# Kernel optimization log

Hardware: AMD Instinct MI355X
Metric: run time of the kernel (lower is better)

The kernel has to match this reference:

```python
import jax, jax.numpy as jnp
import numpy as np

GAMMA = 0.5

def smooth_step(t, gamma=GAMMA):
    # DSelect-k SmoothStep: 0 below -g/2, 1 above g/2, cubic in between.
    tc = jnp.clip(t, -gamma / 2, gamma / 2)
    return (-2.0 / gamma**3) * tc**3 + (3.0 / (2.0 * gamma)) * tc + 0.5

def setup_inputs() -> dict:
    key = jax.random.key(0)
    k1, k2, k3 = jax.random.split(key, 3)
    B, p, k, m = 65536, 1024, 8, 6
    x = jax.random.normal(k1, (B, p), dtype=jnp.float32)
    G_w = jax.random.normal(k2, (k, p), dtype=jnp.float32) / np.sqrt(p)
    G_b = jnp.zeros((k,), dtype=jnp.float32)
    W_w = jax.random.normal(k3, (k * m, p), dtype=jnp.float32) / np.sqrt(p)
    W_b = jnp.zeros((k * m,), dtype=jnp.float32)
    return {"x": x, "G_w": G_w, "G_b": G_b, "W_w": W_w, "W_b": W_b}

def reference(x, G_w, G_b, W_w, W_b):
    B = x.shape[0]
    k = G_w.shape[0]
    m = W_w.shape[0] // k
    n = 2 ** m  # number of experts encoded by m binary gates
    gates = (x @ W_w.T + W_b).reshape(B, k, m)
    z = smooth_step(gates)  # (B, k, m) in [0, 1]
    # per_example_selector: probability of expert e = prod_j (z_j if bit_j(e) else 1-z_j)
    bits = ((np.arange(n)[:, None] >> np.arange(m)[None, :]) & 1).astype(bool)  # (n, m)
    bits = jnp.asarray(bits)
    sel = jnp.prod(jnp.where(bits[None, None, :, :], z[:, :, None, :], 1.0 - z[:, :, None, :]), axis=-1)  # (B, k, n)
    weights = jax.nn.softmax(x @ G_w.T + G_b, axis=1)  # (B, k)
    mixture = jnp.einsum('bk,bkn->bn', weights, sel)  # bmm((B,1,k),(B,k,n)) -> (B, n)
    return mixture
```

## Files before the change

kernel.cpp:

```cpp
#include <hip/hip_runtime.h>

typedef _Float16 half8 __attribute__((ext_vector_type(8)));
typedef float f32x4 __attribute__((ext_vector_type(4)));
typedef float f4 __attribute__((ext_vector_type(4)));

#define P_DIM 1024
#define BM 64
#define NH 8
#define AF_ROW 132

__global__ __launch_bounds__(256) void prep_weights(
    const float* __restrict__ Gw, const float* __restrict__ Gb,
    const float* __restrict__ Ww, const float* __restrict__ Wb,
    _Float16* __restrict__ Wf2, float* __restrict__ biasC) {
  int i = blockIdx.x * 256 + threadIdx.x;
  int j = i & 7;
  int l = (i >> 3) & 63;
  int t = (i >> 9) & 3;
  int S = i >> 11;
  int row = t * 16 + (l & 15);
  int k   = S * 32 + (l >> 4) * 8 + j;
  float v = 0.0f;
  if (row < 48) v = Ww[row * P_DIM + k];
  else if (row < 56) v = Gw[(row - 48) * P_DIM + k];
  Wf2[i] = (_Float16)v;
  if (i < 64) {
    float bv = 0.0f;
    if (i < 48) bv = Wb[i];
    else if (i < 56) bv = Gb[i - 48];
    biasC[i] = bv;
  }
}

#define LOAD_B(dst, c) do { const char* p_ = bg + (size_t)(c) * 8192; \
    dst[0] = *(const half8*)(p_);          dst[1] = *(const half8*)(p_ + 4096); \
    dst[2] = *(const half8*)(p_ + 1024);   dst[3] = *(const half8*)(p_ + 5120); \
    dst[4] = *(const half8*)(p_ + 2048);   dst[5] = *(const half8*)(p_ + 6144); \
    dst[6] = *(const half8*)(p_ + 3072);   dst[7] = *(const half8*)(p_ + 7168); \
  } while (0)

#define BODY(bX, cc) do { \
    f4 aX[4]; \
    { const char* p_ = Abase + (cc) * 256; \
      aX[0] = *(const f4*)(p_);       aX[1] = *(const f4*)(p_ + 16); \
      aX[2] = *(const f4*)(p_ + 128); aX[3] = *(const f4*)(p_ + 144); } \
    half8 h0_, h1_; \
    h0_[0]=(_Float16)aX[0][0]; h0_[1]=(_Float16)aX[0][1]; h0_[2]=(_Float16)aX[0][2]; h0_[3]=(_Float16)aX[0][3]; \
    h0_[4]=(_Float16)aX[1][0]; h0_[5]=(_Float16)aX[1][1]; h0_[6]=(_Float16)aX[1][2]; h0_[7]=(_Float16)aX[1][3]; \
    h1_[0]=(_Float16)aX[2][0]; h1_[1]=(_Float16)aX[2][1]; h1_[2]=(_Float16)aX[2][2]; h1_[3]=(_Float16)aX[2][3]; \
    h1_[4]=(_Float16)aX[3][0]; h1_[5]=(_Float16)aX[3][1]; h1_[6]=(_Float16)aX[3][2]; h1_[7]=(_Float16)aX[3][3]; \
    acc[0] = __builtin_amdgcn_mfma_f32_16x16x32_f16(h0_, bX[0], acc[0], 0, 0, 0); \
    acc[0] = __builtin_amdgcn_mfma_f32_16x16x32_f16(h1_, bX[1], acc[0], 0, 0, 0); \
    acc[1] = __builtin_amdgcn_mfma_f32_16x16x32_f16(h0_, bX[2], acc[1], 0, 0, 0); \
    acc[1] = __builtin_amdgcn_mfma_f32_16x16x32_f16(h1_, bX[3], acc[1], 0, 0, 0); \
    acc[2] = __builtin_amdgcn_mfma_f32_16x16x32_f16(h0_, bX[4], acc[2], 0, 0, 0); \
    acc[2] = __builtin_amdgcn_mfma_f32_16x16x32_f16(h1_, bX[5], acc[2], 0, 0, 0); \
    acc[3] = __builtin_amdgcn_mfma_f32_16x16x32_f16(h0_, bX[6], acc[3], 0, 0, 0); \
    acc[3] = __builtin_amdgcn_mfma_f32_16x16x32_f16(h1_, bX[7], acc[3], 0, 0, 0); \
  } while (0)

__global__ __launch_bounds__(256, 3) void fused_gate(
    const float* __restrict__ x, const _Float16* __restrict__ Wf2,
    const float* __restrict__ biasC, float* __restrict__ out) {
  __shared__ __align__(16) float Af[BM][AF_ROW];

  const int tid  = threadIdx.x;
  const int lane = tid & 63;
  const int w    = tid >> 6;
  const int row0 = blockIdx.x * BM;
  const int l15  = lane & 15;
  const int q    = lane >> 4;

  const char* xg = (const char*)(x + (size_t)(row0 + w * 16) * P_DIM) + lane * 8;
  const char* bg = (const char*)Wf2 + lane * 16;

  char* Aw = (char*)&Af[w * 16][0] + lane * 8;
  const char* Abase = (const char*)&Af[w * 16 + l15][0] + q * 32;

  f32x4 acc[4];
#pragma unroll
  for (int t = 0; t < 4; ++t) acc[t] = (f32x4){0.f, 0.f, 0.f, 0.f};

  float2 pf[16];
#pragma unroll
  for (int i = 0; i < 16; ++i) pf[i] = *(const float2*)(xg + i * 4096);

  half8 bA[8], bB[8];
  LOAD_B(bA, 0);

  for (int h = 0; h < NH; ++h) {
#pragma unroll
    for (int i = 0; i < 16; ++i)
      *(float2*)(Aw + i * 528) = pf[i];
    const int c0 = h * 2;
    LOAD_B(bB, c0 + 1);
    if (h + 1 < NH) {
#pragma unroll
      for (int i = 0; i < 16; ++i)
        pf[i] = *(const float2*)(xg + i * 4096 + (h + 1) * 512);
    }
    BODY(bA, 0);
    BODY(bB, 1);
    if (h + 1 < NH)
      LOAD_B(bA, c0 + 2);
  }

  __syncthreads();
  float (*S)[65] = (float (*)[65])&Af[0][0];

#pragma unroll
  for (int t = 0; t < 4; ++t) {
    float bias = biasC[16 * t + l15];
#pragma unroll
    for (int rr = 0; rr < 4; ++rr) {
      S[w * 16 + q * 4 + rr][16 * t + l15] = acc[t][rr] + bias;
    }
  }
  __syncthreads();

  const int r2  = tid >> 2;
  const int sub = tid & 3;

  float lg[8];
#pragma unroll
  for (int k = 0; k < 8; ++k) lg[k] = S[r2][48 + k];
  float mx = lg[0];
#pragma unroll
  for (int k = 1; k < 8; ++k) mx = fmaxf(mx, lg[k]);
  float wk[8];
  float ssum = 0.f;
#pragma unroll
  for (int k = 0; k < 8; ++k) { wk[k] = expf(lg[k] - mx); ssum += wk[k]; }
  const float inv = 1.0f / ssum;

  float mix[16];
#pragma unroll
  for (int i = 0; i < 16; ++i) mix[i] = 0.f;

#pragma unroll
  for (int k = 0; k < 8; ++k) {
    float z[6];
#pragma unroll
    for (int j = 0; j < 6; ++j) {
      float tt = S[r2][k * 6 + j];
      float tc = fminf(fmaxf(tt, -0.25f), 0.25f);
      z[j] = fmaf(tc, fmaf(-16.0f * tc, tc, 3.0f), 0.5f);
    }
    float f4v = (sub & 1) ? z[4] : 1.0f - z[4];
    float f5v = (sub & 2) ? z[5] : 1.0f - z[5];
    float wf = wk[k] * inv * f4v * f5v;
    float t2[2], t4[4], t8[8], t16[16];
    t2[0] = 1.0f - z[0]; t2[1] = z[0];
#pragma unroll
    for (int i = 0; i < 2; ++i) { t4[i] = t2[i] * (1.0f - z[1]); t4[i + 2] = t2[i] * z[1]; }
#pragma unroll
    for (int i = 0; i < 4; ++i) { t8[i] = t4[i] * (1.0f - z[2]); t8[i + 4] = t4[i] * z[2]; }
#pragma unroll
    for (int i = 0; i < 8; ++i) { t16[i] = t8[i] * (1.0f - z[3]); t16[i + 8] = t8[i] * z[3]; }
#pragma unroll
    for (int i = 0; i < 16; ++i) mix[i] = fmaf(wf, t16[i], mix[i]);
  }

  float* op = out + (size_t)(row0 + r2) * 64 + sub * 16;
#pragma unroll
  for (int g = 0; g < 4; ++g) {
    float4 o;
    o.x = mix[4 * g + 0]; o.y = mix[4 * g + 1];
    o.z = mix[4 * g + 2]; o.w = mix[4 * g + 3];
    ((float4*)op)[g] = o;
  }
}

extern "C" void kernel_launch(void* const* d_in, const int* in_sizes, int n_in,
                              void* d_out, int out_size, void* d_ws, size_t ws_size,
                              hipStream_t stream) {
  const float* x  = (const float*)d_in[0];
  const float* Gw = (const float*)d_in[1];
  const float* Gb = (const float*)d_in[2];
  const float* Ww = (const float*)d_in[3];
  const float* Wb = (const float*)d_in[4];
  float* out = (float*)d_out;

  _Float16* Wf2  = (_Float16*)d_ws;
  float*    bias = (float*)((char*)d_ws + 64 * P_DIM * sizeof(_Float16));

  const int B = in_sizes[0] / P_DIM;

  prep_weights<<<dim3(256), dim3(256), 0, stream>>>(Gw, Gb, Ww, Wb, Wf2, bias);
  fused_gate<<<dim3(B / BM), dim3(256), 0, stream>>>(x, Wf2, bias, out);
  (void)n_in; (void)out_size; (void)ws_size;
}
```

Before: 66.08 us.

## Retile MFMA work to 2x2 wave grid of 32x32 output tiles

Each wave now computes a 32-row by 32-column output tile instead of 16 rows by all 64 columns, halving per-wave B-fragment register loads and sharing A tiles across waves through LDS. Because waves now read rows written by other waves, two __syncthreads per K-chunk are added around the LDS staging. This lowers register pressure and global/L2 traffic for weights, at the cost of extra block-level barriers and more LDS reads with fp16 conversion per wave.

After: 58.43 us. -11.6%, faster.

```diff
diff --git a/kernel.cpp b/kernel.cpp
--- a/kernel.cpp
+++ b/kernel.cpp
@@ -32,31 +32,36 @@
   }
 }
 
-#define LOAD_B(dst, c) do { const char* p_ = bg + (size_t)(c) * 8192; \
+#define LOAD_B(dst, c) do { const char* p_ = bgw + (size_t)(c) * 8192; \
     dst[0] = *(const half8*)(p_);          dst[1] = *(const half8*)(p_ + 4096); \
     dst[2] = *(const half8*)(p_ + 1024);   dst[3] = *(const half8*)(p_ + 5120); \
-    dst[4] = *(const half8*)(p_ + 2048);   dst[5] = *(const half8*)(p_ + 6144); \
-    dst[6] = *(const half8*)(p_ + 3072);   dst[7] = *(const half8*)(p_ + 7168); \
   } while (0)
 
 #define BODY(bX, cc) do { \
-    f4 aX[4]; \
-    { const char* p_ = Abase + (cc) * 256; \
-      aX[0] = *(const f4*)(p_);       aX[1] = *(const f4*)(p_ + 16); \
-      aX[2] = *(const f4*)(p_ + 128); aX[3] = *(const f4*)(p_ + 144); } \
-    half8 h0_, h1_; \
-    h0_[0]=(_Float16)aX[0][0]; h0_[1]=(_Float16)aX[0][1]; h0_[2]=(_Float16)aX[0][2]; h0_[3]=(_Float16)aX[0][3]; \
-    h0_[4]=(_Float16)aX[1][0]; h0_[5]=(_Float16)aX[1][1]; h0_[6]=(_Float16)aX[1][2]; h0_[7]=(_Float16)aX[1][3]; \
-    h1_[0]=(_Float16)aX[2][0]; h1_[1]=(_Float16)aX[2][1]; h1_[2]=(_Float16)aX[2][2]; h1_[3]=(_Float16)aX[2][3]; \
-    h1_[4]=(_Float16)aX[3][0]; h1_[5]=(_Float16)aX[3][1]; h1_[6]=(_Float16)aX[3][2]; h1_[7]=(_Float16)aX[3][3]; \
-    acc[0] = __builtin_amdgcn_mfma_f32_16x16x32_f16(h0_, bX[0], acc[0], 0, 0, 0); \
-    acc[0] = __builtin_amdgcn_mfma_f32_16x16x32_f16(h1_, bX[1], acc[0], 0, 0, 0); \
-    acc[1] = __builtin_amdgcn_mfma_f32_16x16x32_f16(h0_, bX[2], acc[1], 0, 0, 0); \
-    acc[1] = __builtin_amdgcn_mfma_f32_16x16x32_f16(h1_, bX[3], acc[1], 0, 0, 0); \
-    acc[2] = __builtin_amdgcn_mfma_f32_16x16x32_f16(h0_, bX[4], acc[2], 0, 0, 0); \
-    acc[2] = __builtin_amdgcn_mfma_f32_16x16x32_f16(h1_, bX[5], acc[2], 0, 0, 0); \
-    acc[3] = __builtin_amdgcn_mfma_f32_16x16x32_f16(h0_, bX[6], acc[3], 0, 0, 0); \
-    acc[3] = __builtin_amdgcn_mfma_f32_16x16x32_f16(h1_, bX[7], acc[3], 0, 0, 0); \
+    f4 a0_[4], a1_[4]; \
+    { const char* p0 = Abase0 + (cc) * 256; \
+      a0_[0] = *(const f4*)(p0);       a0_[1] = *(const f4*)(p0 + 16); \
+      a0_[2] = *(const f4*)(p0 + 128); a0_[3] = *(const f4*)(p0 + 144); \
+      const char* p1 = Abase1 + (cc) * 256; \
+      a1_[0] = *(const f4*)(p1);       a1_[1] = *(const f4*)(p1 + 16); \
+      a1_[2] = *(const f4*)(p1 + 128); a1_[3] = *(const f4*)(p1 + 144); } \
+    half8 h00_, h01_, h10_, h11_; \
+    h00_[0]=(_Float16)a0_[0][0]; h00_[1]=(_Float16)a0_[0][1]; h00_[2]=(_Float16)a0_[0][2]; h00_[3]=(_Float16)a0_[0][3]; \
+    h00_[4]=(_Float16)a0_[1][0]; h00_[5]=(_Float16)a0_[1][1]; h00_[6]=(_Float16)a0_[1][2]; h00_[7]=(_Float16)a0_[1][3]; \
+    h01_[0]=(_Float16)a0_[2][0]; h01_[1]=(_Float16)a0_[2][1]; h01_[2]=(_Float16)a0_[2][2]; h01_[3]=(_Float16)a0_[2][3]; \
+    h01_[4]=(_Float16)a0_[3][0]; h01_[5]=(_Float16)a0_[3][1]; h01_[6]=(_Float16)a0_[3][2]; h01_[7]=(_Float16)a0_[3][3]; \
+    h10_[0]=(_Float16)a1_[0][0]; h10_[1]=(_Float16)a1_[0][1]; h10_[2]=(_Float16)a1_[0][2]; h10_[3]=(_Float16)a1_[0][3]; \
+    h10_[4]=(_Float16)a1_[1][0]; h10_[5]=(_Float16)a1_[1][1]; h10_[6]=(_Float16)a1_[1][2]; h10_[7]=(_Float16)a1_[1][3]; \
+    h11_[0]=(_Float16)a1_[2][0]; h11_[1]=(_Float16)a1_[2][1]; h11_[2]=(_Float16)a1_[2][2]; h11_[3]=(_Float16)a1_[2][3]; \
+    h11_[4]=(_Float16)a1_[3][0]; h11_[5]=(_Float16)a1_[3][1]; h11_[6]=(_Float16)a1_[3][2]; h11_[7]=(_Float16)a1_[3][3]; \
+    acc[0] = __builtin_amdgcn_mfma_f32_16x16x32_f16(h00_, bX[0], acc[0], 0, 0, 0); \
+    acc[0] = __builtin_amdgcn_mfma_f32_16x16x32_f16(h01_, bX[1], acc[0], 0, 0, 0); \
+    acc[1] = __builtin_amdgcn_mfma_f32_16x16x32_f16(h00_, bX[2], acc[1], 0, 0, 0); \
+    acc[1] = __builtin_amdgcn_mfma_f32_16x16x32_f16(h01_, bX[3], acc[1], 0, 0, 0); \
+    acc[2] = __builtin_amdgcn_mfma_f32_16x16x32_f16(h10_, bX[0], acc[2], 0, 0, 0); \
+    acc[2] = __builtin_amdgcn_mfma_f32_16x16x32_f16(h11_, bX[1], acc[2], 0, 0, 0); \
+    acc[3] = __builtin_amdgcn_mfma_f32_16x16x32_f16(h10_, bX[2], acc[3], 0, 0, 0); \
+    acc[3] = __builtin_amdgcn_mfma_f32_16x16x32_f16(h11_, bX[3], acc[3], 0, 0, 0); \
   } while (0)
 
 __global__ __launch_bounds__(256, 3) void fused_gate(
@@ -71,11 +76,15 @@
   const int l15  = lane & 15;
   const int q    = lane >> 4;
 
+  const int mrow = (w >> 1) * 32;
+  const int ncol = (w & 1) * 32;
+
   const char* xg = (const char*)(x + (size_t)(row0 + w * 16) * P_DIM) + lane * 8;
-  const char* bg = (const char*)Wf2 + lane * 16;
+  const char* bgw = (const char*)Wf2 + lane * 16 + (size_t)(ncol / 16) * 1024;
 
   char* Aw = (char*)&Af[w * 16][0] + lane * 8;
-  const char* Abase = (const char*)&Af[w * 16 + l15][0] + q * 32;
+  const char* Abase0 = (const char*)&Af[mrow + l15][0] + q * 32;
+  const char* Abase1 = Abase0 + 16 * 528;
 
   f32x4 acc[4];
 #pragma unroll
@@ -85,13 +94,15 @@
 #pragma unroll
   for (int i = 0; i < 16; ++i) pf[i] = *(const float2*)(xg + i * 4096);
 
-  half8 bA[8], bB[8];
+  half8 bA[4], bB[4];
   LOAD_B(bA, 0);
 
   for (int h = 0; h < NH; ++h) {
+    if (h) __syncthreads();
 #pragma unroll
     for (int i = 0; i < 16; ++i)
       *(float2*)(Aw + i * 528) = pf[i];
+    __syncthreads();
     const int c0 = h * 2;
     LOAD_B(bB, c0 + 1);
     if (h + 1 < NH) {
@@ -109,11 +120,15 @@
   float (*S)[65] = (float (*)[65])&Af[0][0];
 
 #pragma unroll
-  for (int t = 0; t < 4; ++t) {
-    float bias = biasC[16 * t + l15];
-#pragma unroll
-    for (int rr = 0; rr < 4; ++rr) {
-      S[w * 16 + q * 4 + rr][16 * t + l15] = acc[t][rr] + bias;
+  for (int m = 0; m < 2; ++m) {
+#pragma unroll
+    for (int j = 0; j < 2; ++j) {
+      const int col = ncol + j * 16 + l15;
+      float bias = biasC[col];
+#pragma unroll
+      for (int rr = 0; rr < 4; ++rr) {
+        S[mrow + m * 16 + q * 4 + rr][col] = acc[m * 2 + j][rr] + bias;
+      }
     }
   }
   __syncthreads();
```
